# Kernel tuning notes

Measured on AMD Instinct MI355X. Metric: run time of the kernel, lower is better.

The kernel has to match this reference:

```python
import jax, jax.numpy as jnp
import numpy as np
from jax import lax

B, T, F, H, NC = 64, 256, 64, 128, 2


def setup_inputs() -> dict:
    key = jax.random.key(0)
    ks = jax.random.split(key, 10)
    # timestamps: sorted ints with duplicates -> exercises per-timestamp mean aggregation
    t = jnp.sort(jax.random.randint(ks[0], (B, T), 0, T // 2), axis=1).astype(jnp.float32)
    m = jax.random.randint(ks[1], (B, T), 0, F).astype(jnp.float32)
    x = jax.random.normal(ks[2], (B, T), dtype=jnp.float32)
    delt = jax.random.uniform(ks[3], (B, T), dtype=jnp.float32)
    X = jnp.stack([t, m, x, delt], axis=1)  # [B, 4, T]
    lengths = jax.random.randint(ks[4], (B,), T // 2, T + 1).astype(jnp.int32)
    s = 1.0 / np.sqrt(H + 1)
    W_lin = jax.random.uniform(ks[5], (F, H + 1, 4 * H), minval=-s, maxval=s, dtype=jnp.float32)
    b_lin = jax.random.uniform(ks[6], (F, 4 * H), minval=-s, maxval=s, dtype=jnp.float32)
    W_dec = jax.random.uniform(ks[7], (F,), minval=-1.0, maxval=1.0, dtype=jnp.float32)
    b_dec = jax.random.uniform(ks[8], (F,), minval=-1.0, maxval=1.0, dtype=jnp.float32)
    so = 1.0 / np.sqrt(F * H + H)
    k9, k10 = jax.random.split(ks[9])
    W_out = jax.random.uniform(k9, (F * H + H, NC), minval=-so, maxval=so, dtype=jnp.float32)
    b_out = jax.random.uniform(k10, (NC,), minval=-so, maxval=so, dtype=jnp.float32)
    return {"X": X, "lengths": lengths, "W_lin": W_lin, "b_lin": b_lin,
            "W_dec": W_dec, "b_dec": b_dec, "W_out": W_out, "b_out": b_out}


def _forward(X, lengths, W_lin, b_lin, W_dec, b_dec, W_out, b_out):
    nF, Hp1, H4 = W_lin.shape
    hs = Hp1 - 1
    t = X[:, 0]
    m = X[:, 1].astype(jnp.int32)
    x = X[:, 2]
    delt = X[:, 3]
    idx = jnp.arange(t.shape[1])
    valid = idx[None, :] < lengths[:, None]                       # event is real
    t_next = jnp.concatenate([t[:, 1:], t[:, -1:] + 1.0], axis=1)
    # last event of a consecutive-equal-timestamp group (within valid length)
    boundary = (idx[None, :] == (lengths[:, None] - 1)) | (t_next != t)

    def per_sample(m_s, x_s, d_s, v_s, b_s):
        def step(carry, inp):
            h_t, c_t, acc, cnt = carry
            mj, xj, dj, vj, bj = inp
            # feature-specific decay of that feature's hidden row
            dm = W_dec[mj] * dj + b_dec[mj]
            decay = jnp.exp(-jnp.maximum(0.0, dm))
            h_dec = decay * h_t[mj]
            inp_vec = jnp.concatenate([xj[None], h_dec])          # [H+1]
            gates = inp_vec @ W_lin[mj] + b_lin[mj]               # [4H]
            gi, gf, go, gc = jnp.split(gates, 4)
            c_cand = jax.nn.sigmoid(gf) * c_t + jax.nn.sigmoid(gi) * jnp.tanh(gc)
            h_row = jax.nn.sigmoid(go) * jnp.tanh(c_cand)
            h_t = jnp.where(vj, h_t.at[mj].set(h_row), h_t)
            acc = acc + jnp.where(vj, c_cand, 0.0)
            cnt = cnt + jnp.where(vj, 1.0, 0.0)
            close = vj & bj                                       # end of timestamp group
            c_t = jnp.where(close, acc / jnp.maximum(cnt, 1.0), c_t)
            acc = jnp.where(close, jnp.zeros_like(acc), acc)
            cnt = jnp.where(close, 0.0, cnt)
            return (h_t, c_t, acc, cnt), None

        init = (jnp.zeros((nF, hs), jnp.float32), jnp.zeros((hs,), jnp.float32),
                jnp.zeros((hs,), jnp.float32), jnp.float32(0.0))
        (h_t, c_t, _, _), _ = lax.scan(step, init, (m_s, x_s, d_s, v_s, b_s))
        feats = jnp.concatenate([c_t, h_t.reshape(-1)])           # [H + F*H]
        return jax.nn.softmax(feats @ W_out + b_out)

    return jax.vmap(per_sample)(m, x, delt, valid, boundary)      # [B, n_class]


def reference(X, lengths, W_lin, b_lin, W_dec, b_dec, W_out, b_out):
    return _forward(X, lengths, W_lin, b_lin, W_dec, b_dec, W_out, b_out)
```

## Files before the change

kernel.cpp:

```cpp
#include <hip/hip_runtime.h>
#include <math.h>
#include <stdint.h>

#define BATCH 64
#define T 256
#define NF 64
#define H 128
#define H4 512
#define HP1 129
#define WF_STRIDE (HP1 * H4)
#define FEATS (NF * H + H)
#define NTH 1024

#define PACK8_U4 (64 * 2 * 2 * 1024)
#define PACK8_BYTES ((size_t)PACK8_U4 * 16u)

typedef float vf2 __attribute__((ext_vector_type(2)));

__device__ __forceinline__ float sigmoidf_(float x) {
    return 1.0f / (1.0f + __expf(-x));
}

__device__ __forceinline__ float tanhf_(float x) {
    float ax = fabsf(x);
    float e = __expf(2.0f * ax);
    float r = 1.0f - 2.0f / (e + 1.0f);
    return copysignf(r, x);
}

template<bool HI>
__device__ __forceinline__ vf2 dec2f(unsigned u) {
    return __builtin_amdgcn_cvt_pk_f32_fp8(u, HI);
}

__global__ __launch_bounds__(256)
void repack8_kernel(const float* __restrict__ W_lin, uint4* __restrict__ pack) {
    const int lin = blockIdx.x * 256 + threadIdx.x;
    const int tid = lin & 1023;
    const int q   = (lin >> 10) & 1;
    const int h   = (lin >> 11) & 1;
    const int f   = lin >> 12;
    const int kh  = tid >> 9;
    const int cc  = tid & 511;
    const int k0  = h * 64 + kh * 32 + q * 16;
    const float* src = W_lin + (size_t)f * WF_STRIDE + (size_t)(1 + k0) * H4 + cc;
    unsigned u[4];
    #pragma unroll
    for (int w = 0; w < 4; ++w) {
        const float v0 = src[(4 * w + 0) * H4] * 4096.0f;
        const float v1 = src[(4 * w + 1) * H4] * 4096.0f;
        const float v2 = src[(4 * w + 2) * H4] * 4096.0f;
        const float v3 = src[(4 * w + 3) * H4] * 4096.0f;
        unsigned r = 0;
        r = __builtin_amdgcn_cvt_pk_fp8_f32(v0, v1, r, false);
        r = __builtin_amdgcn_cvt_pk_fp8_f32(v2, v3, r, true);
        u[w] = r;
    }
    uint4 o; o.x = u[0]; o.y = u[1]; o.z = u[2]; o.w = u[3];
    pack[lin] = o;
}

__global__ __launch_bounds__(NTH, 2)
void lstm_scan_fp8_v2(const float* __restrict__ X,
                      const int* __restrict__ lengths,
                      const float* __restrict__ W_lin,
                      const float* __restrict__ b_lin,
                      const float* __restrict__ W_dec,
                      const float* __restrict__ b_dec,
                      const float* __restrict__ W_out,
                      const float* __restrict__ b_out,
                      const uint4* __restrict__ pack,
                      float* __restrict__ out)
{
    __shared__ float s_feats[FEATS];
    __shared__ float s_inp[H];
    __shared__ float s_part[2][H4];
    __shared__ float s_X[4 * T];
    __shared__ float s_wdec[NF];
    __shared__ float s_bdec[NF];
    __shared__ float s_red[32];

    float* s_ct = s_feats;
    float* s_ht = s_feats + H;

    const int tid = threadIdx.x;
    const int b   = blockIdx.x;
    const int c   = tid & 511;
    const int kh  = tid >> 9;

    const float* Xb = X + b * 4 * T;
    const int len = lengths[b];

    for (int i = tid; i < NF * H; i += NTH) s_ht[i] = 0.0f;
    for (int i = tid; i < 4 * T; i += NTH) s_X[i] = Xb[i];
    if (tid < NF) { s_wdec[tid] = W_dec[tid]; s_bdec[tid] = b_dec[tid]; }
    if (tid < H) s_inp[tid] = 0.0f;
    __syncthreads();

    float c_t = 0.0f, accs = 0.0f, cnts = 0.0f;

    #define DOTF(W, K0) do {                                                    \
        const vf2* ip = (const vf2*)(s_inp + (K0));                             \
        vf2 d;                                                                  \
        d = dec2f<false>((W).x); acc += d * ip[0];                              \
        d = dec2f<true >((W).x); acc += d * ip[1];                              \
        d = dec2f<false>((W).y); acc += d * ip[2];                              \
        d = dec2f<true >((W).y); acc += d * ip[3];                              \
        d = dec2f<false>((W).z); acc += d * ip[4];                              \
        d = dec2f<true >((W).z); acc += d * ip[5];                              \
        d = dec2f<false>((W).w); acc += d * ip[6];                              \
        d = dec2f<true >((W).w); acc += d * ip[7];                              \
    } while (0)

    uint4 A0, A1, A2, A3, B0, B1, B2, B3;
    float4 blA = make_float4(0.f, 0.f, 0.f, 0.f), blB = make_float4(0.f, 0.f, 0.f, 0.f);
    float  wxA = 0.0f, wxB = 0.0f;

    {
        const int m0 = (int)s_X[T];
        const uint4* p0 = pack + (size_t)m0 * 4096 + tid;
        A0 = p0[0]; A1 = p0[1024]; A2 = p0[2048]; A3 = p0[3072];
        if (tid < H) {
            const float* bb = b_lin + m0 * H4 + tid;
            blA.x = bb[0]; blA.y = bb[H]; blA.z = bb[2 * H]; blA.w = bb[3 * H];
        }
        if (kh == 0) wxA = W_lin[(size_t)m0 * WF_STRIDE + c];
    }

    #define STEP(C0, C1, C2, C3, N0, N1, N2, N3, CBL, NBL, CWX, NWX)            \
    {                                                                           \
        const int   mj  = (int)s_X[T + j];                                      \
        const float xj  = s_X[2 * T + j];                                       \
        const int   jn  = (j + 1 < T) ? (j + 1) : (T - 1);                      \
        const int   mjn = (int)s_X[T + jn];                                     \
        \
        {                                                                       \
            const uint4* pn = pack + (size_t)mjn * 4096 + tid;                  \
            N0 = pn[0]; N1 = pn[1024]; N2 = pn[2048]; N3 = pn[3072];            \
        }                                                                       \
        if (tid < H) {                                                          \
            const float* bb = b_lin + mjn * H4 + tid;                           \
            NBL.x = bb[0]; NBL.y = bb[H]; NBL.z = bb[2 * H]; NBL.w = bb[3 * H]; \
        }                                                                       \
        if (kh == 0) NWX = W_lin[(size_t)mjn * WF_STRIDE + c];                  \
           \
        vf2 acc; acc[0] = 0.0f; acc[1] = 0.0f;                                  \
        DOTF(C0, kh * 32);                                                      \
        DOTF(C1, kh * 32 + 16);                                                 \
        DOTF(C2, 64 + kh * 32);                                                 \
        DOTF(C3, 64 + kh * 32 + 16);                                            \
        float a = (acc[0] + acc[1]) * (1.0f / 4096.0f);                         \
        if (kh == 0) a = fmaf(xj, CWX, a);                                      \
        s_part[kh][c] = a;                                                      \
        __syncthreads();                                 \
        if (tid < H) {                                                          \
            const int h = tid;                                                  \
            const float gi = s_part[0][h]       + s_part[1][h]       + CBL.x;   \
            const float gf = s_part[0][H + h]   + s_part[1][H + h]   + CBL.y;   \
            const float go = s_part[0][2*H + h] + s_part[1][2*H + h] + CBL.z;   \
            const float gc = s_part[0][3*H + h] + s_part[1][3*H + h] + CBL.w;   \
            const float c_cand = sigmoidf_(gf) * c_t + sigmoidf_(gi) * tanhf_(gc); \
            const float h_row  = sigmoidf_(go) * tanhf_(c_cand);                \
            s_ht[mj * H + h] = h_row;                                           \
            accs += c_cand;                                                     \
            cnts += 1.0f;                                                       \
            const float tj = s_X[j];                                            \
            const float tn = (j < T - 1) ? s_X[j + 1] : (tj + 1.0f);            \
            const bool boundary = (j == len - 1) || (tn != tj);                 \
            if (boundary) { c_t = accs / fmaxf(cnts, 1.0f); accs = 0.0f; cnts = 0.0f; } \
                                   \
            const float dn  = s_X[3 * T + jn];                                  \
            const float dmn = fmaf(s_wdec[mjn], dn, s_bdec[mjn]);               \
            const float den = __expf(-fmaxf(0.0f, dmn));                        \
            const float hv  = (mjn == mj) ? h_row : s_ht[mjn * H + h];          \
            s_inp[h] = den * hv;                                                \
        }                                                                       \
        __syncthreads();                              \
    }

    int j = 0;
    while (j < len) {
        STEP(A0, A1, A2, A3, B0, B1, B2, B3, blA, blB, wxA, wxB); ++j;
        if (j >= len) break;
        STEP(B0, B1, B2, B3, A0, A1, A2, A3, blB, blA, wxB, wxA); ++j;
    }
    #undef STEP
    #undef DOTF

    if (tid < H) s_ct[tid] = c_t;
    __syncthreads();

    float z0 = 0.0f, z1 = 0.0f;
    for (int i = tid; i < FEATS; i += NTH) {
        const float f = s_feats[i];
        const float2 w = *(const float2*)(W_out + 2 * i);
        z0 = fmaf(f, w.x, z0);
        z1 = fmaf(f, w.y, z1);
    }
    #pragma unroll
    for (int off = 32; off > 0; off >>= 1) {
        z0 += __shfl_down(z0, off, 64);
        z1 += __shfl_down(z1, off, 64);
    }
    const int wave = tid >> 6, lane = tid & 63;
    if (lane == 0) { s_red[2 * wave] = z0; s_red[2 * wave + 1] = z1; }
    __syncthreads();
    if (tid == 0) {
        float a0 = b_out[0], a1 = b_out[1];
        #pragma unroll
        for (int w = 0; w < 16; ++w) { a0 += s_red[2 * w]; a1 += s_red[2 * w + 1]; }
        const float mx = fmaxf(a0, a1);
        const float e0 = __expf(a0 - mx), e1 = __expf(a1 - mx);
        const float inv = 1.0f / (e0 + e1);
        out[2 * b]     = e0 * inv;
        out[2 * b + 1] = e1 * inv;
    }
}

#define NTHREADS 512
__global__ __launch_bounds__(NTHREADS)
void lstm_scan_kernel(const float* __restrict__ X,
                      const int* __restrict__ lengths,
                      const float* __restrict__ W_lin,
                      const float* __restrict__ b_lin,
                      const float* __restrict__ W_dec,
                      const float* __restrict__ b_dec,
                      const float* __restrict__ W_out,
                      const float* __restrict__ b_out,
                      float* __restrict__ out)
{
    __shared__ float s_feats[FEATS];
    __shared__ float s_inp[H];
    __shared__ float s_part[4][H4];
    __shared__ float s_X[4 * T];
    __shared__ float s_wdec[NF];
    __shared__ float s_bdec[NF];
    __shared__ float s_red[16];

    float* s_ct = s_feats;
    float* s_ht = s_feats + H;

    const int tid = threadIdx.x;
    const int b   = blockIdx.x;
    const int g4  = tid & 127;
    const int kq  = tid >> 7;

    const float* Xb = X + b * 4 * T;
    const int len = lengths[b];

    for (int i = tid; i < NF * H; i += NTHREADS) s_ht[i] = 0.0f;
    for (int i = tid; i < 4 * T; i += NTHREADS) s_X[i] = Xb[i];
    if (tid < NF) { s_wdec[tid] = W_dec[tid]; s_bdec[tid] = b_dec[tid]; }
    __syncthreads();

    float c_t = 0.0f, acc = 0.0f, cnt = 0.0f;

    for (int j = 0; j < len; ++j) {
        const int   mj = (int)s_X[T + j];
        const float xj = s_X[2 * T + j];
        const float* Wf = W_lin + mj * WF_STRIDE;

        float bl0, bl1, bl2, bl3;
        if (tid < H) {
            const float dj    = s_X[3 * T + j];
            const float dm    = fmaf(s_wdec[mj], dj, s_bdec[mj]);
            const float decay = __expf(-fmaxf(0.0f, dm));
            s_inp[tid] = decay * s_ht[mj * H + tid];
            const int m4 = mj * H4;
            bl0 = b_lin[m4 + tid];
            bl1 = b_lin[m4 + H + tid];
            bl2 = b_lin[m4 + 2 * H + tid];
            bl3 = b_lin[m4 + 3 * H + tid];
        }
        __syncthreads();

        float4 a4 = make_float4(0.0f, 0.0f, 0.0f, 0.0f);
        {
            const float*  wr  = Wf + (1 + kq * 32) * H4 + 4 * g4;
            const float4* ivp = (const float4*)(s_inp + kq * 32);
            #pragma unroll
            for (int cc = 0; cc < 8; ++cc) {
                const float4 v = ivp[cc];
                const float* wrc = wr + (4 * cc) * H4;
                const float4 w0 = *(const float4*)(wrc);
                const float4 w1 = *(const float4*)(wrc + H4);
                const float4 w2 = *(const float4*)(wrc + 2 * H4);
                const float4 w3 = *(const float4*)(wrc + 3 * H4);
                a4.x = fmaf(v.x, w0.x, a4.x); a4.y = fmaf(v.x, w0.y, a4.y);
                a4.z = fmaf(v.x, w0.z, a4.z); a4.w = fmaf(v.x, w0.w, a4.w);
                a4.x = fmaf(v.y, w1.x, a4.x); a4.y = fmaf(v.y, w1.y, a4.y);
                a4.z = fmaf(v.y, w1.z, a4.z); a4.w = fmaf(v.y, w1.w, a4.w);
                a4.x = fmaf(v.z, w2.x, a4.x); a4.y = fmaf(v.z, w2.y, a4.y);
                a4.z = fmaf(v.z, w2.z, a4.z); a4.w = fmaf(v.z, w2.w, a4.w);
                a4.x = fmaf(v.w, w3.x, a4.x); a4.y = fmaf(v.w, w3.y, a4.y);
                a4.z = fmaf(v.w, w3.z, a4.z); a4.w = fmaf(v.w, w3.w, a4.w);
            }
        }
        if (kq == 0) {
            const float4 wv = *(const float4*)(Wf + 4 * g4);
            a4.x = fmaf(xj, wv.x, a4.x); a4.y = fmaf(xj, wv.y, a4.y);
            a4.z = fmaf(xj, wv.z, a4.z); a4.w = fmaf(xj, wv.w, a4.w);
        }
        *(float4*)(&s_part[kq][4 * g4]) = a4;
        __syncthreads();

        if (tid < H) {
            const int h = tid;
            const float gi = s_part[0][h]         + s_part[1][h]         + s_part[2][h]         + s_part[3][h]         + bl0;
            const float gf = s_part[0][H + h]     + s_part[1][H + h]     + s_part[2][H + h]     + s_part[3][H + h]     + bl1;
            const float go = s_part[0][2*H + h]   + s_part[1][2*H + h]   + s_part[2][2*H + h]   + s_part[3][2*H + h]   + bl2;
            const float gc = s_part[0][3*H + h]   + s_part[1][3*H + h]   + s_part[2][3*H + h]   + s_part[3][3*H + h]   + bl3;

            const float c_cand = sigmoidf_(gf) * c_t + sigmoidf_(gi) * tanhf_(gc);
            const float h_row  = sigmoidf_(go) * tanhf_(c_cand);
            s_ht[mj * H + h] = h_row;
            acc += c_cand;
            cnt += 1.0f;

            const float tj = s_X[j];
            const float tn = (j < T - 1) ? s_X[j + 1] : (tj + 1.0f);
            const bool boundary = (j == len - 1) || (tn != tj);
            if (boundary) { c_t = acc / fmaxf(cnt, 1.0f); acc = 0.0f; cnt = 0.0f; }
        }
        __syncthreads();
    }

    if (tid < H) s_ct[tid] = c_t;
    __syncthreads();

    float z0 = 0.0f, z1 = 0.0f;
    for (int i = tid; i < FEATS; i += NTHREADS) {
        const float f = s_feats[i];
        const float2 wv = *(const float2*)(W_out + 2 * i);
        z0 = fmaf(f, wv.x, z0);
        z1 = fmaf(f, wv.y, z1);
    }
    #pragma unroll
    for (int off = 32; off > 0; off >>= 1) {
        z0 += __shfl_down(z0, off, 64);
        z1 += __shfl_down(z1, off, 64);
    }
    const int wave = tid >> 6, lane = tid & 63;
    if (lane == 0) { s_red[2 * wave] = z0; s_red[2 * wave + 1] = z1; }
    __syncthreads();
    if (tid == 0) {
        float a0 = b_out[0], a1 = b_out[1];
        #pragma unroll
        for (int q = 0; q < 8; ++q) { a0 += s_red[2 * q]; a1 += s_red[2 * q + 1]; }
        const float mx = fmaxf(a0, a1);
        const float e0 = __expf(a0 - mx), e1 = __expf(a1 - mx);
        const float inv = 1.0f / (e0 + e1);
        out[2 * b]     = e0 * inv;
        out[2 * b + 1] = e1 * inv;
    }
}

extern "C" void kernel_launch(void* const* d_in, const int* in_sizes, int n_in,
                              void* d_out, int out_size, void* d_ws, size_t ws_size,
                              hipStream_t stream) {
    const float* X      = (const float*)d_in[0];
    const int*   lens   = (const int*)d_in[1];
    const float* W_lin  = (const float*)d_in[2];
    const float* b_lin  = (const float*)d_in[3];
    const float* W_dec  = (const float*)d_in[4];
    const float* b_dec  = (const float*)d_in[5];
    const float* W_out  = (const float*)d_in[6];
    const float* b_out  = (const float*)d_in[7];
    float* out = (float*)d_out;

    if (ws_size >= PACK8_BYTES) {
        uint4* pack = (uint4*)d_ws;
        hipLaunchKernelGGL(repack8_kernel, dim3(PACK8_U4 / 256), dim3(256), 0, stream,
                           W_lin, pack);
        hipLaunchKernelGGL(lstm_scan_fp8_v2, dim3(BATCH), dim3(NTH), 0, stream,
                           X, lens, W_lin, b_lin, W_dec, b_dec, W_out, b_out, pack, out);
    } else {
        hipLaunchKernelGGL(lstm_scan_kernel, dim3(BATCH), dim3(NTHREADS), 0, stream,
                           X, lens, W_lin, b_lin, W_dec, b_dec, W_out, b_out, out);
    }
}
```

Baseline: 448.8 us.

## Pack per-thread weights, input column and bias into contiguous 80-byte records

```diff
diff --git a/kernel.cpp b/kernel.cpp
--- a/kernel.cpp
+++ b/kernel.cpp
@@ -12,8 +12,7 @@
 #define FEATS (NF * H + H)
 #define NTH 1024
 
-#define PACK8_U4 (64 * 2 * 2 * 1024)
-#define PACK8_BYTES ((size_t)PACK8_U4 * 16u)
+#define REC_BYTES ((size_t)NF * 1024 * 80)
 
 typedef float vf2 __attribute__((ext_vector_type(2)));
 
@@ -33,43 +32,63 @@
     return __builtin_amdgcn_cvt_pk_f32_fp8(u, HI);
 }
 
+#define WAITV(N) do { asm volatile("s_waitcnt vmcnt(" #N ")" ::: "memory"); \
+                      __builtin_amdgcn_sched_barrier(0); } while (0)
+#define BARRIER() do { asm volatile("s_waitcnt lgkmcnt(0)" ::: "memory"); \
+                       __builtin_amdgcn_s_barrier(); \
+                       asm volatile("" ::: "memory"); } while (0)
+
 __global__ __launch_bounds__(256)
-void repack8_kernel(const float* __restrict__ W_lin, uint4* __restrict__ pack) {
+void repack5_kernel(const float* __restrict__ W_lin, const float* __restrict__ b_lin,
+                    uint4* __restrict__ rec) {
     const int lin = blockIdx.x * 256 + threadIdx.x;
     const int tid = lin & 1023;
-    const int q   = (lin >> 10) & 1;
-    const int h   = (lin >> 11) & 1;
-    const int f   = lin >> 12;
+    const int f   = lin >> 10;
     const int kh  = tid >> 9;
     const int cc  = tid & 511;
-    const int k0  = h * 64 + kh * 32 + q * 16;
-    const float* src = W_lin + (size_t)f * WF_STRIDE + (size_t)(1 + k0) * H4 + cc;
-    unsigned u[4];
+    uint4* orec = rec + (size_t)lin * 5;
     #pragma unroll
-    for (int w = 0; w < 4; ++w) {
-        const float v0 = src[(4 * w + 0) * H4] * 4096.0f;
-        const float v1 = src[(4 * w + 1) * H4] * 4096.0f;
-        const float v2 = src[(4 * w + 2) * H4] * 4096.0f;
-        const float v3 = src[(4 * w + 3) * H4] * 4096.0f;
-        unsigned r = 0;
-        r = __builtin_amdgcn_cvt_pk_fp8_f32(v0, v1, r, false);
-        r = __builtin_amdgcn_cvt_pk_fp8_f32(v2, v3, r, true);
-        u[w] = r;
-    }
-    uint4 o; o.x = u[0]; o.y = u[1]; o.z = u[2]; o.w = u[3];
-    pack[lin] = o;
+    for (int i = 0; i < 4; ++i) {
+        const int h  = i >> 1;
+        const int q  = i & 1;
+        const int k0 = h * 64 + kh * 32 + q * 16;
+        const float* src = W_lin + (size_t)f * WF_STRIDE + (size_t)(1 + k0) * H4 + cc;
+        unsigned u[4];
+        #pragma unroll
+        for (int w = 0; w < 4; ++w) {
+            const float v0 = src[(4 * w + 0) * H4] * 4096.0f;
+            const float v1 = src[(4 * w + 1) * H4] * 4096.0f;
+            const float v2 = src[(4 * w + 2) * H4] * 4096.0f;
+            const float v3 = src[(4 * w + 3) * H4] * 4096.0f;
+            unsigned r = 0;
+            r = __builtin_amdgcn_cvt_pk_fp8_f32(v0, v1, r, false);
+            r = __builtin_amdgcn_cvt_pk_fp8_f32(v2, v3, r, true);
+            u[w] = r;
+        }
+        uint4 o; o.x = u[0]; o.y = u[1]; o.z = u[2]; o.w = u[3];
+        orec[i] = o;
+    }
+    union { uint4 u; float fv[4]; _Float16 hf[8]; } hd;
+    hd.u = make_uint4(0, 0, 0, 0);
+    hd.fv[0] = (kh == 0) ? W_lin[(size_t)f * WF_STRIDE + cc] : 0.0f;
+    if (tid < H) {
+        const float* bb = b_lin + f * H4 + tid;
+        hd.hf[2] = (_Float16)bb[0];
+        hd.hf[3] = (_Float16)bb[H];
+        hd.hf[4] = (_Float16)bb[2 * H];
+        hd.hf[5] = (_Float16)bb[3 * H];
+    }
+    orec[4] = hd.u;
 }
 
 __global__ __launch_bounds__(NTH, 2)
-void lstm_scan_fp8_v2(const float* __restrict__ X,
+void lstm_scan_fp8_v3(const float* __restrict__ X,
                       const int* __restrict__ lengths,
-                      const float* __restrict__ W_lin,
-                      const float* __restrict__ b_lin,
                       const float* __restrict__ W_dec,
                       const float* __restrict__ b_dec,
                       const float* __restrict__ W_out,
                       const float* __restrict__ b_out,
-                      const uint4* __restrict__ pack,
+                      const uint4* __restrict__ rec,
                       float* __restrict__ out)
 {
     __shared__ float s_feats[FEATS];
@@ -98,6 +117,18 @@
     __syncthreads();
 
     float c_t = 0.0f, accs = 0.0f, cnts = 0.0f;
+
+    #define ISSUE5(MF, R0, R1, R2, R3, R4) do {                                 \
+        const uint64_t ap = (uint64_t)(uintptr_t)((const char*)rec              \
+                          + ((size_t)(MF) * 1024 + tid) * 80);                  \
+        asm volatile("global_load_dwordx4 %0, %5, off\n\t"                      \
+                     "global_load_dwordx4 %1, %5, off offset:16\n\t"            \
+                     "global_load_dwordx4 %2, %5, off offset:32\n\t"            \
+                     "global_load_dwordx4 %3, %5, off offset:48\n\t"            \
+                     "global_load_dwordx4 %4, %5, off offset:64"                \
+                     : "=&v"(R0), "=&v"(R1), "=&v"(R2), "=&v"(R3), "=&v"(R4)    \
+                     : "v"(ap) : "memory");                                     \
+    } while (0)
 
     #define DOTF(W, K0) do {                                                    \
         const vf2* ip = (const vf2*)(s_inp + (K0));                             \
@@ -112,53 +143,37 @@
         d = dec2f<true >((W).w); acc += d * ip[7];                              \
     } while (0)
 
-    uint4 A0, A1, A2, A3, B0, B1, B2, B3;
-    float4 blA = make_float4(0.f, 0.f, 0.f, 0.f), blB = make_float4(0.f, 0.f, 0.f, 0.f);
-    float  wxA = 0.0f, wxB = 0.0f;
+    uint4 A0, A1, A2, A3, AH, B0, B1, B2, B3, BH;
 
     {
         const int m0 = (int)s_X[T];
-        const uint4* p0 = pack + (size_t)m0 * 4096 + tid;
-        A0 = p0[0]; A1 = p0[1024]; A2 = p0[2048]; A3 = p0[3072];
-        if (tid < H) {
-            const float* bb = b_lin + m0 * H4 + tid;
-            blA.x = bb[0]; blA.y = bb[H]; blA.z = bb[2 * H]; blA.w = bb[3 * H];
-        }
-        if (kh == 0) wxA = W_lin[(size_t)m0 * WF_STRIDE + c];
-    }
-
-    #define STEP(C0, C1, C2, C3, N0, N1, N2, N3, CBL, NBL, CWX, NWX)            \
+        ISSUE5(m0, A0, A1, A2, A3, AH);
+    }
+
+    #define STEP(C0, C1, C2, C3, CH, N0, N1, N2, N3, NH)                        \
     {                                                                           \
         const int   mj  = (int)s_X[T + j];                                      \
         const float xj  = s_X[2 * T + j];                                       \
         const int   jn  = (j + 1 < T) ? (j + 1) : (T - 1);                      \
         const int   mjn = (int)s_X[T + jn];                                     \
-        \
-        {                                                                       \
-            const uint4* pn = pack + (size_t)mjn * 4096 + tid;                  \
-            N0 = pn[0]; N1 = pn[1024]; N2 = pn[2048]; N3 = pn[3072];            \
-        }                                                                       \
-        if (tid < H) {                                                          \
-            const float* bb = b_lin + mjn * H4 + tid;                           \
-            NBL.x = bb[0]; NBL.y = bb[H]; NBL.z = bb[2 * H]; NBL.w = bb[3 * H]; \
-        }                                                                       \
-        if (kh == 0) NWX = W_lin[(size_t)mjn * WF_STRIDE + c];                  \
-           \
+        ISSUE5(mjn, N0, N1, N2, N3, NH);                      \
+        WAITV(5);                                  \
         vf2 acc; acc[0] = 0.0f; acc[1] = 0.0f;                                  \
         DOTF(C0, kh * 32);                                                      \
         DOTF(C1, kh * 32 + 16);                                                 \
         DOTF(C2, 64 + kh * 32);                                                 \
         DOTF(C3, 64 + kh * 32 + 16);                                            \
+        union { uint4 u; float fv[4]; _Float16 hf[8]; } hu; hu.u = CH;          \
         float a = (acc[0] + acc[1]) * (1.0f / 4096.0f);                         \
-        if (kh == 0) a = fmaf(xj, CWX, a);                                      \
+        if (kh == 0) a = fmaf(xj, hu.fv[0], a);                                 \
         s_part[kh][c] = a;                                                      \
-        __syncthreads();                                 \
+        BARRIER();                   \
         if (tid < H) {                                                          \
             const int h = tid;                                                  \
-            const float gi = s_part[0][h]       + s_part[1][h]       + CBL.x;   \
-            const float gf = s_part[0][H + h]   + s_part[1][H + h]   + CBL.y;   \
-            const float go = s_part[0][2*H + h] + s_part[1][2*H + h] + CBL.z;   \
-            const float gc = s_part[0][3*H + h] + s_part[1][3*H + h] + CBL.w;   \
+            const float gi = s_part[0][h]       + s_part[1][h]       + (float)hu.hf[2]; \
+            const float gf = s_part[0][H + h]   + s_part[1][H + h]   + (float)hu.hf[3]; \
+            const float go = s_part[0][2*H + h] + s_part[1][2*H + h] + (float)hu.hf[4]; \
+            const float gc = s_part[0][3*H + h] + s_part[1][3*H + h] + (float)hu.hf[5]; \
             const float c_cand = sigmoidf_(gf) * c_t + sigmoidf_(gi) * tanhf_(gc); \
             const float h_row  = sigmoidf_(go) * tanhf_(c_cand);                \
             s_ht[mj * H + h] = h_row;                                           \
@@ -168,24 +183,27 @@
             const float tn = (j < T - 1) ? s_X[j + 1] : (tj + 1.0f);            \
             const bool boundary = (j == len - 1) || (tn != tj);                 \
             if (boundary) { c_t = accs / fmaxf(cnts, 1.0f); accs = 0.0f; cnts = 0.0f; } \
-                                   \
             const float dn  = s_X[3 * T + jn];                                  \
             const float dmn = fmaf(s_wdec[mjn], dn, s_bdec[mjn]);               \
             const float den = __expf(-fmaxf(0.0f, dmn));                        \
             const float hv  = (mjn == mj) ? h_row : s_ht[mjn * H + h];          \
             s_inp[h] = den * hv;                                                \
         }                                                                       \
-        __syncthreads();                              \
+        BARRIER();                                    \
     }
 
     int j = 0;
     while (j < len) {
-        STEP(A0, A1, A2, A3, B0, B1, B2, B3, blA, blB, wxA, wxB); ++j;
+        STEP(A0, A1, A2, A3, AH, B0, B1, B2, B3, BH); ++j;
         if (j >= len) break;
-        STEP(B0, B1, B2, B3, A0, A1, A2, A3, blB, blA, wxB, wxA); ++j;
+        STEP(B0, B1, B2, B3, BH, A0, A1, A2, A3, AH); ++j;
     }
     #undef STEP
     #undef DOTF
+    #undef ISSUE5
+
+    asm volatile("s_waitcnt vmcnt(0) lgkmcnt(0)" ::: "memory");
+    __syncthreads();
 
     if (tid < H) s_ct[tid] = c_t;
     __syncthreads();
@@ -368,12 +386,12 @@
     const float* b_out  = (const float*)d_in[7];
     float* out = (float*)d_out;
 
-    if (ws_size >= PACK8_BYTES) {
-        uint4* pack = (uint4*)d_ws;
-        hipLaunchKernelGGL(repack8_kernel, dim3(PACK8_U4 / 256), dim3(256), 0, stream,
-                           W_lin, pack);
-        hipLaunchKernelGGL(lstm_scan_fp8_v2, dim3(BATCH), dim3(NTH), 0, stream,
-                           X, lens, W_lin, b_lin, W_dec, b_dec, W_out, b_out, pack, out);
+    if (ws_size >= REC_BYTES) {
+        uint4* rec = (uint4*)d_ws;
+        hipLaunchKernelGGL(repack5_kernel, dim3(NF * 1024 / 256), dim3(256), 0, stream,
+                           W_lin, b_lin, rec);
+        hipLaunchKernelGGL(lstm_scan_fp8_v3, dim3(BATCH), dim3(NTH), 0, stream,
+                           X, lens, W_dec, b_dec, W_out, b_out, rec, out);
     } else {
         hipLaunchKernelGGL(lstm_scan_kernel, dim3(BATCH), dim3(NTHREADS), 0, stream,
                            X, lens, W_lin, b_lin, W_dec, b_dec, W_out, b_out, out);
```

After: 458.2 us. 2.1% more time.

## Split recurrent dot over 8 k-slices with 4 gates per thread

Applied to the files above, without the earlier changes.

```diff
diff --git a/kernel.cpp b/kernel.cpp
--- a/kernel.cpp
+++ b/kernel.cpp
@@ -12,8 +12,10 @@
 #define FEATS (NF * H + H)
 #define NTH 1024
 
-#define PACK8_U4 (64 * 2 * 2 * 1024)
-#define PACK8_BYTES ((size_t)PACK8_U4 * 16u)
+#define PACK_U4 (NF * 4 * 1024)
+#define PACK_BYTES ((size_t)PACK_U4 * 16u)
+#define AUX_BYTES ((size_t)NF * 1024 * 16u)
+#define WS_NEED (PACK_BYTES + AUX_BYTES)
 
 typedef float vf2 __attribute__((ext_vector_type(2)));
 
@@ -34,23 +36,23 @@
 }
 
 __global__ __launch_bounds__(256)
-void repack8_kernel(const float* __restrict__ W_lin, uint4* __restrict__ pack) {
+void repack6_kernel(const float* __restrict__ W_lin, uint4* __restrict__ pack) {
     const int lin = blockIdx.x * 256 + threadIdx.x;
-    const int tid = lin & 1023;
-    const int q   = (lin >> 10) & 1;
-    const int h   = (lin >> 11) & 1;
+    const int t   = lin & 1023;
+    const int i   = (lin >> 10) & 3;
     const int f   = lin >> 12;
-    const int kh  = tid >> 9;
-    const int cc  = tid & 511;
-    const int k0  = h * 64 + kh * 32 + q * 16;
-    const float* src = W_lin + (size_t)f * WF_STRIDE + (size_t)(1 + k0) * H4 + cc;
+    const int kq  = t >> 7;
+    const int cg  = t & 127;
+    const int col = i * 128 + cg;
     unsigned u[4];
     #pragma unroll
     for (int w = 0; w < 4; ++w) {
-        const float v0 = src[(4 * w + 0) * H4] * 4096.0f;
-        const float v1 = src[(4 * w + 1) * H4] * 4096.0f;
-        const float v2 = src[(4 * w + 2) * H4] * 4096.0f;
-        const float v3 = src[(4 * w + 3) * H4] * 4096.0f;
+        const float* src = W_lin + (size_t)f * WF_STRIDE
+                         + (size_t)(1 + kq * 16 + 4 * w) * H4 + col;
+        const float v0 = src[0]      * 4096.0f;
+        const float v1 = src[H4]     * 4096.0f;
+        const float v2 = src[2 * H4] * 4096.0f;
+        const float v3 = src[3 * H4] * 4096.0f;
         unsigned r = 0;
         r = __builtin_amdgcn_cvt_pk_fp8_f32(v0, v1, r, false);
         r = __builtin_amdgcn_cvt_pk_fp8_f32(v2, v3, r, true);
@@ -60,21 +62,43 @@
     pack[lin] = o;
 }
 
+__global__ __launch_bounds__(256)
+void aux6_kernel(const float* __restrict__ W_lin, const float* __restrict__ b_lin,
+                 float4* __restrict__ aux) {
+    const int lin = blockIdx.x * 256 + threadIdx.x;
+    const int t   = lin & 1023;
+    const int f   = lin >> 10;
+    const int kq  = t >> 7;
+    const int cg  = t & 127;
+    float4 o = make_float4(0.f, 0.f, 0.f, 0.f);
+    if (kq == 0) {
+        o.x = W_lin[(size_t)f * WF_STRIDE + cg];
+        o.y = W_lin[(size_t)f * WF_STRIDE + 128 + cg];
+        o.z = W_lin[(size_t)f * WF_STRIDE + 256 + cg];
+        o.w = W_lin[(size_t)f * WF_STRIDE + 384 + cg];
+    } else if (kq == 1) {
+        o.x = b_lin[f * H4 + cg];
+        o.y = b_lin[f * H4 + 128 + cg];
+        o.z = b_lin[f * H4 + 256 + cg];
+        o.w = b_lin[f * H4 + 384 + cg];
+    }
+    aux[lin] = o;
+}
+
 __global__ __launch_bounds__(NTH, 2)
-void lstm_scan_fp8_v2(const float* __restrict__ X,
+void lstm_scan_fp8_v4(const float* __restrict__ X,
                       const int* __restrict__ lengths,
-                      const float* __restrict__ W_lin,
-                      const float* __restrict__ b_lin,
                       const float* __restrict__ W_dec,
                       const float* __restrict__ b_dec,
                       const float* __restrict__ W_out,
                       const float* __restrict__ b_out,
                       const uint4* __restrict__ pack,
+                      const float4* __restrict__ aux,
                       float* __restrict__ out)
 {
     __shared__ float s_feats[FEATS];
     __shared__ float s_inp[H];
-    __shared__ float s_part[2][H4];
+    __shared__ float s_part[8][H4];
     __shared__ float s_X[4 * T];
     __shared__ float s_wdec[NF];
     __shared__ float s_bdec[NF];
@@ -85,8 +109,8 @@
 
     const int tid = threadIdx.x;
     const int b   = blockIdx.x;
-    const int c   = tid & 511;
-    const int kh  = tid >> 9;
+    const int cg  = tid & 127;
+    const int kq  = tid >> 7;
 
     const float* Xb = X + b * 4 * T;
     const int len = lengths[b];
@@ -99,68 +123,81 @@
 
     float c_t = 0.0f, accs = 0.0f, cnts = 0.0f;
 
-    #define DOTF(W, K0) do {                                                    \
-        const vf2* ip = (const vf2*)(s_inp + (K0));                             \
+    #define DOTC(W, ACC) do {                                                   \
         vf2 d;                                                                  \
-        d = dec2f<false>((W).x); acc += d * ip[0];                              \
-        d = dec2f<true >((W).x); acc += d * ip[1];                              \
-        d = dec2f<false>((W).y); acc += d * ip[2];                              \
-        d = dec2f<true >((W).y); acc += d * ip[3];                              \
-        d = dec2f<false>((W).z); acc += d * ip[4];                              \
-        d = dec2f<true >((W).z); acc += d * ip[5];                              \
-        d = dec2f<false>((W).w); acc += d * ip[6];                              \
-        d = dec2f<true >((W).w); acc += d * ip[7];                              \
+        d = dec2f<false>((W).x); ACC += d * iv8[0];                             \
+        d = dec2f<true >((W).x); ACC += d * iv8[1];                             \
+        d = dec2f<false>((W).y); ACC += d * iv8[2];                             \
+        d = dec2f<true >((W).y); ACC += d * iv8[3];                             \
+        d = dec2f<false>((W).z); ACC += d * iv8[4];                             \
+        d = dec2f<true >((W).z); ACC += d * iv8[5];                             \
+        d = dec2f<false>((W).w); ACC += d * iv8[6];                             \
+        d = dec2f<true >((W).w); ACC += d * iv8[7];                             \
     } while (0)
 
     uint4 A0, A1, A2, A3, B0, B1, B2, B3;
-    float4 blA = make_float4(0.f, 0.f, 0.f, 0.f), blB = make_float4(0.f, 0.f, 0.f, 0.f);
-    float  wxA = 0.0f, wxB = 0.0f;
+    float4 AX = make_float4(0.f, 0.f, 0.f, 0.f), BX = AX;
 
     {
         const int m0 = (int)s_X[T];
         const uint4* p0 = pack + (size_t)m0 * 4096 + tid;
         A0 = p0[0]; A1 = p0[1024]; A2 = p0[2048]; A3 = p0[3072];
-        if (tid < H) {
-            const float* bb = b_lin + m0 * H4 + tid;
-            blA.x = bb[0]; blA.y = bb[H]; blA.z = bb[2 * H]; blA.w = bb[3 * H];
-        }
-        if (kh == 0) wxA = W_lin[(size_t)m0 * WF_STRIDE + c];
-    }
-
-    #define STEP(C0, C1, C2, C3, N0, N1, N2, N3, CBL, NBL, CWX, NWX)            \
+        AX = aux[(size_t)m0 * 1024 + tid];
+    }
+
+    #define STEP(C0, C1, C2, C3, CX, N0, N1, N2, N3, NX)                        \
     {                                                                           \
         const int   mj  = (int)s_X[T + j];                                      \
         const float xj  = s_X[2 * T + j];                                       \
         const int   jn  = (j + 1 < T) ? (j + 1) : (T - 1);                      \
         const int   mjn = (int)s_X[T + jn];                                     \
-        \
+                              \
         {                                                                       \
             const uint4* pn = pack + (size_t)mjn * 4096 + tid;                  \
             N0 = pn[0]; N1 = pn[1024]; N2 = pn[2048]; N3 = pn[3072];            \
+            NX = aux[(size_t)mjn * 1024 + tid];                                 \
         }                                                                       \
-        if (tid < H) {                                                          \
-            const float* bb = b_lin + mjn * H4 + tid;                           \
-            NBL.x = bb[0]; NBL.y = bb[H]; NBL.z = bb[2 * H]; NBL.w = bb[3 * H]; \
+           \
+        vf2 iv8[8];                                                             \
+        {                                                                       \
+            const float4* ip = (const float4*)(s_inp + kq * 16);                \
+            _Pragma("unroll")                                                   \
+            for (int q = 0; q < 4; ++q) {                                       \
+                const float4 t_ = ip[q];                                        \
+                iv8[2 * q][0] = t_.x;     iv8[2 * q][1] = t_.y;                 \
+                iv8[2 * q + 1][0] = t_.z; iv8[2 * q + 1][1] = t_.w;             \
+            }                                                                   \
         }                                                                       \
-        if (kh == 0) NWX = W_lin[(size_t)mjn * WF_STRIDE + c];                  \
-           \
-        vf2 acc; acc[0] = 0.0f; acc[1] = 0.0f;                                  \
-        DOTF(C0, kh * 32);                                                      \
-        DOTF(C1, kh * 32 + 16);                                                 \
-        DOTF(C2, 64 + kh * 32);                                                 \
-        DOTF(C3, 64 + kh * 32 + 16);                                            \
-        float a = (acc[0] + acc[1]) * (1.0f / 4096.0f);                         \
-        if (kh == 0) a = fmaf(xj, CWX, a);                                      \
-        s_part[kh][c] = a;                                                      \
+        vf2 ac0, ac1, ac2, ac3;                                                 \
+        ac0 = 0.0f; ac1 = 0.0f; ac2 = 0.0f; ac3 = 0.0f;                         \
+        DOTC(C0, ac0); DOTC(C1, ac1); DOTC(C2, ac2); DOTC(C3, ac3);             \
+        float a0 = (ac0[0] + ac0[1]) * (1.0f / 4096.0f);                        \
+        float a1 = (ac1[0] + ac1[1]) * (1.0f / 4096.0f);                        \
+        float a2 = (ac2[0] + ac2[1]) * (1.0f / 4096.0f);                        \
+        float a3 = (ac3[0] + ac3[1]) * (1.0f / 4096.0f);                        \
+        if (kq == 0) {                                                          \
+            a0 = fmaf(xj, CX.x, a0); a1 = fmaf(xj, CX.y, a1);                   \
+            a2 = fmaf(xj, CX.z, a2); a3 = fmaf(xj, CX.w, a3);                   \
+        } else if (kq == 1) {                                                   \
+            a0 += CX.x; a1 += CX.y; a2 += CX.z; a3 += CX.w;                     \
+        }                                                                       \
+        s_part[kq][cg]       = a0;                                              \
+        s_part[kq][128 + cg] = a1;                                              \
+        s_part[kq][256 + cg] = a2;                                              \
+        s_part[kq][384 + cg] = a3;                                              \
         __syncthreads();                                 \
         if (tid < H) {                                                          \
             const int h = tid;                                                  \
-            const float gi = s_part[0][h]       + s_part[1][h]       + CBL.x;   \
-            const float gf = s_part[0][H + h]   + s_part[1][H + h]   + CBL.y;   \
-            const float go = s_part[0][2*H + h] + s_part[1][2*H + h] + CBL.z;   \
-            const float gc = s_part[0][3*H + h] + s_part[1][3*H + h] + CBL.w;   \
-            const float c_cand = sigmoidf_(gf) * c_t + sigmoidf_(gi) * tanhf_(gc); \
-            const float h_row  = sigmoidf_(go) * tanhf_(c_cand);                \
+            float g0 = 0.f, g1 = 0.f, g2 = 0.f, g3 = 0.f;                       \
+            _Pragma("unroll")                                                   \
+            for (int q = 0; q < 8; ++q) {                                       \
+                g0 += s_part[q][h];                                             \
+                g1 += s_part[q][128 + h];                                       \
+                g2 += s_part[q][256 + h];                                       \
+                g3 += s_part[q][384 + h];                                       \
+            }                                                                   \
+            const float c_cand = sigmoidf_(g1) * c_t + sigmoidf_(g0) * tanhf_(g3); \
+            const float h_row  = sigmoidf_(g2) * tanhf_(c_cand);                \
             s_ht[mj * H + h] = h_row;                                           \
             accs += c_cand;                                                     \
             cnts += 1.0f;                                                       \
@@ -168,7 +205,6 @@
             const float tn = (j < T - 1) ? s_X[j + 1] : (tj + 1.0f);            \
             const bool boundary = (j == len - 1) || (tn != tj);                 \
             if (boundary) { c_t = accs / fmaxf(cnts, 1.0f); accs = 0.0f; cnts = 0.0f; } \
-                                   \
             const float dn  = s_X[3 * T + jn];                                  \
             const float dmn = fmaf(s_wdec[mjn], dn, s_bdec[mjn]);               \
             const float den = __expf(-fmaxf(0.0f, dmn));                        \
@@ -180,12 +216,12 @@
 
     int j = 0;
     while (j < len) {
-        STEP(A0, A1, A2, A3, B0, B1, B2, B3, blA, blB, wxA, wxB); ++j;
+        STEP(A0, A1, A2, A3, AX, B0, B1, B2, B3, BX); ++j;
         if (j >= len) break;
-        STEP(B0, B1, B2, B3, A0, A1, A2, A3, blB, blA, wxB, wxA); ++j;
+        STEP(B0, B1, B2, B3, BX, A0, A1, A2, A3, AX); ++j;
     }
     #undef STEP
-    #undef DOTF
+    #undef DOTC
 
     if (tid < H) s_ct[tid] = c_t;
     __syncthreads();
@@ -368,12 +404,15 @@
     const float* b_out  = (const float*)d_in[7];
     float* out = (float*)d_out;
 
-    if (ws_size >= PACK8_BYTES) {
-        uint4* pack = (uint4*)d_ws;
-        hipLaunchKernelGGL(repack8_kernel, dim3(PACK8_U4 / 256), dim3(256), 0, stream,
+    if (ws_size >= WS_NEED) {
+        uint4*  pack = (uint4*)d_ws;
+        float4* aux  = (float4*)((char*)d_ws + PACK_BYTES);
+        hipLaunchKernelGGL(repack6_kernel, dim3(PACK_U4 / 256), dim3(256), 0, stream,
                            W_lin, pack);
-        hipLaunchKernelGGL(lstm_scan_fp8_v2, dim3(BATCH), dim3(NTH), 0, stream,
-                           X, lens, W_lin, b_lin, W_dec, b_dec, W_out, b_out, pack, out);
+        hipLaunchKernelGGL(aux6_kernel, dim3(NF * 1024 / 256), dim3(256), 0, stream,
+                           W_lin, b_lin, aux);
+        hipLaunchKernelGGL(lstm_scan_fp8_v4, dim3(BATCH), dim3(NTH), 0, stream,
+                           X, lens, W_dec, b_dec, W_out, b_out, pack, aux, out);
     } else {
         hipLaunchKernelGGL(lstm_scan_kernel, dim3(BATCH), dim3(NTHREADS), 0, stream,
                            X, lens, W_lin, b_lin, W_dec, b_dec, W_out, b_out, out);
```

After: 448.7 us. No clear change (-0.0%).
